# Performance work log

Measured on AMD Instinct MI355X. Metric: run time of the kernel, lower is better.

## Reference

```python
import jax, jax.numpy as jnp
import numpy as np
from jax import lax

MODES = 16
DEPTH = 8
NPH = 8  # photons = sum(init_state); init_state = [1]*8 + [0]*8
IDX = np.arange(NPH)  # output_indices derived from init_state
PI = np.pi
CHUNK = 4096  # pairs per permanent chunk (memory control, mirrors chunk_subsets idea)


def setup_inputs() -> dict:
    key = jax.random.key(0)
    k1, k2, k3 = jax.random.split(key, 3)
    x = jax.random.normal(k1, (256, 64), dtype=jnp.float32)
    W = jax.random.normal(k2, (120, 64), dtype=jnp.float32) / np.sqrt(64.0)
    b = jax.random.normal(k3, (120,), dtype=jnp.float32) * 0.01
    return {"x": x, "W": W, "b": b}


def _forward(x, W, b):
    N = x.shape[0]
    # fc1 + sigmoid embedding -> angle pairs
    x_emb = jax.nn.sigmoid(x @ W.T + b)              # (N, 120)
    tbu = x_emb.reshape(N, -1, 2)                    # (N, T, 2)
    theta = tbu[:, :, 0] * (PI / 2)
    phi = tbu[:, :, 1] * (2 * PI)
    ct = jnp.cos(theta).astype(jnp.complex64)
    st = jnp.sin(theta).astype(jnp.complex64)
    ep = jnp.exp(1j * phi.astype(jnp.complex64))
    # 2x2 tunable beam-splitter unitaries: [[e^{i phi} c, -s], [e^{i phi} s, c]]
    row0 = jnp.stack([ep * ct, -st], axis=-1)
    row1 = jnp.stack([ep * st, ct], axis=-1)
    blocks = jnp.stack([row0, row1], axis=-2)        # (N, T, 2, 2)

    # Apply block-diagonal layers. Block-diag matmul only mixes row pairs,
    # so update row segments directly instead of building (modes,modes) UBS.
    U = jnp.broadcast_to(jnp.eye(MODES, dtype=jnp.complex64), (N, MODES, MODES))
    nb_even, nb_odd = MODES // 2, (MODES - 2) // 2
    n_before = 0
    for d in range(DEPTH):
        if d % 2 == 0:
            nb, off = nb_even, 0
        else:
            nb, off = nb_odd, 1
        blk = blocks[:, n_before:n_before + nb]                      # (N, nb, 2, 2)
        seg = U[:, off:off + 2 * nb, :].reshape(N, nb, 2, MODES)     # row pairs
        new = jnp.einsum('nkab,nkbm->nkam', blk, seg).reshape(N, 2 * nb, MODES)
        U = U.at[:, off:off + 2 * nb, :].set(new)
        n_before += nb

    # Photonic Gram: K[a,b] = |perm( (U_a^dag U_b)[idx, idx] )|^2.
    # Only the idx-columns of U enter: V = U[:, :, idx], submatrix = V_a^dag V_b.
    V = U[:, :, IDX]                                  # (N, MODES, n)
    G = jnp.einsum('ami,bmj->abij', V.conj(), V)      # (N, N, n, n)

    n = NPH
    subsets = jnp.arange(1, 1 << n)                   # (S,), S = 2^n - 1
    masks = (subsets[:, None] >> jnp.arange(n)[None, :]) & 1   # (S, n)
    signs = (1 - 2 * ((n - masks.sum(axis=1)) & 1)).astype(jnp.complex64)
    maskc = masks.astype(jnp.complex64)

    A = G.reshape(N * N, n, n)
    nc = (N * N) // CHUNK

    def perm_chunk(Ac):  # Ryser: sum_S (-1)^{n-|S|} prod_i sum_{j in S} A_ij
        ss = jnp.einsum('cij,sj->csi', Ac, maskc)     # (c, S, n) subset row-sums
        pr = jnp.prod(ss, axis=2)                     # (c, S)
        return jnp.sum(pr * signs, axis=1)            # (c,)

    perms = lax.map(perm_chunk, A.reshape(nc, CHUNK, n, n)).reshape(N * N)
    K = (jnp.abs(perms) ** 2).astype(jnp.float32).reshape(N, N)
    di = jnp.arange(N)
    K = K.at[di, di].set(1.0)
    return x_emb, K


def reference(x, W, b):
    return _forward(x, W, b)
```

## Files before the change

kernel.cpp:

```cpp
#include <hip/hip_runtime.h>
#include <math.h>

#define NS 256
#define EMB 120
#define NBLK 60
#define MODES 16
#define NPH 8

typedef float v2f __attribute__((ext_vector_type(2)));

__device__ __forceinline__ v2f cmul(v2f a, v2f b) {
    v2f axx = {a.x, a.x};
    v2f nyy = {-a.y, a.y};
    v2f byx = {b.y, b.x};
    return axx * b + nyy * byx;
}
__device__ __forceinline__ v2f cfma_conj(v2f a, v2f b, v2f c) {
    v2f axx = {a.x, a.x};
    v2f pyy = {a.y, -a.y};
    v2f byx = {b.y, b.x};
    return axx * b + (pyy * byx + c);
}

__global__ __launch_bounds__(128) void emb_v_kernel(
    const float* __restrict__ x, const float* __restrict__ W,
    const float* __restrict__ bias, float* __restrict__ out_emb,
    float2* __restrict__ Vws)
{
    const int s = blockIdx.x;
    const int t = threadIdx.x;
    __shared__ float emb[EMB];
    __shared__ float ctA[NBLK], stA[NBLK], exA[NBLK], eyA[NBLK];

    if (t < EMB) {
        const float* xr = x + s * 64;
        const float* wr = W + t * 64;
        float acc = bias[t];
        #pragma unroll
        for (int k = 0; k < 64; ++k) acc = fmaf(xr[k], wr[k], acc);
        float e = 1.0f / (1.0f + expf(-acc));
        emb[t] = e;
        out_emb[s * EMB + t] = e;
    }
    __syncthreads();

    if (t < NBLK) {
        float th = emb[2 * t]     * 1.57079632679489662f;
        float ph = emb[2 * t + 1] * 6.28318530717958648f;
        float st, ct, sp, cp;
        sincosf(th, &st, &ct);
        sincosf(ph, &sp, &cp);
        ctA[t] = ct; stA[t] = st; exA[t] = cp; eyA[t] = sp;
    }
    __syncthreads();

    if (t < NPH) {
        const int c = t;
        float2 u[MODES];
        #pragma unroll
        for (int m = 0; m < MODES; ++m) {
            u[m].x = (m == c) ? 1.0f : 0.0f;
            u[m].y = 0.0f;
        }
        int bi = 0;
        #pragma unroll
        for (int d = 0; d < 8; ++d) {
            const int off = d & 1;
            const int nb = 8 - off;
            #pragma unroll
            for (int k = 0; k < nb; ++k) {
                float ct = ctA[bi], st = stA[bi], ex = exA[bi], ey = eyA[bi];
                ++bi;
                const int r0 = off + 2 * k;
                float2 u0 = u[r0], u1 = u[r0 + 1];
                float2 n0, n1;
                n0.x = ex * ct * u0.x - ey * ct * u0.y - st * u1.x;
                n0.y = ex * ct * u0.y + ey * ct * u0.x - st * u1.y;
                n1.x = ex * st * u0.x - ey * st * u0.y + ct * u1.x;
                n1.y = ex * st * u0.y + ey * st * u0.x + ct * u1.y;
                u[r0] = n0; u[r0 + 1] = n1;
            }
        }
        #pragma unroll
        for (int m = 0; m < MODES; ++m)
            Vws[(s * MODES + m) * NPH + c] = u[m];
    }
}

__global__ __launch_bounds__(256, 2) void perm_kernel(
    const float2* __restrict__ Vws, float* __restrict__ outK)
{
    __shared__ char smem[64 * 66 * sizeof(float2)];
    float2 (*sva)[132] = (float2(*)[132])smem;
    float2 (*svb)[132] = (float2(*)[132])(smem + 8448);
    float2 (*sG)[66]   = (float2(*)[66])smem;

    const int tid = threadIdx.x;
    const int ta = blockIdx.x >> 5;
    const int tb = blockIdx.x & 31;

    const float4* srcA = (const float4*)(Vws + (size_t)ta * 8 * 128);
    const float4* srcB = (const float4*)(Vws + (size_t)tb * 8 * 128);
    #pragma unroll
    for (int r = 0; r < 2; ++r) {
        int idx = r * 256 + tid;
        int row = idx >> 6;
        int c4  = idx & 63;
        *(float4*)&sva[row][c4 * 2] = srcA[idx];
        *(float4*)&svb[row][c4 * 2] = srcB[idx];
    }
    __syncthreads();

    const int p  = tid >> 2;
    const int q  = tid & 3;
    const int pa = p >> 3;
    const int pb = p & 7;

    v2f Ga[2][8];
    #pragma unroll
    for (int i = 0; i < 2; ++i)
        #pragma unroll
        for (int j = 0; j < 8; ++j) Ga[i][j] = (v2f){0.f, 0.f};

    #pragma unroll 1
    for (int m = 0; m < 16; ++m) {
        float4 va4 = *(const float4*)&sva[pa][m * 8 + 2 * q];
        v2f a0 = {va4.x, va4.y};
        v2f a1 = {va4.z, va4.w};
        v2f vb[8];
        #pragma unroll
        for (int jj = 0; jj < 4; ++jj) {
            float4 b4 = *(const float4*)&svb[pb][m * 8 + 2 * jj];
            vb[2 * jj]     = (v2f){b4.x, b4.y};
            vb[2 * jj + 1] = (v2f){b4.z, b4.w};
        }
        #pragma unroll
        for (int j = 0; j < 8; ++j) {
            Ga[0][j] = cfma_conj(a0, vb[j], Ga[0][j]);
            Ga[1][j] = cfma_conj(a1, vb[j], Ga[1][j]);
        }
    }
    __syncthreads();

    #pragma unroll
    for (int i = 0; i < 2; ++i)
        #pragma unroll
        for (int jj = 0; jj < 4; ++jj) {
            float4 w;
            w.x = Ga[i][2 * jj].x;     w.y = Ga[i][2 * jj].y;
            w.z = Ga[i][2 * jj + 1].x; w.w = Ga[i][2 * jj + 1].y;
            *(float4*)&sG[p][(2 * q + i) * 8 + 2 * jj] = w;
        }
    __syncthreads();

    v2f G[8][8];
    #pragma unroll
    for (int i = 0; i < 8; ++i)
        #pragma unroll
        for (int jj = 0; jj < 4; ++jj) {
            float4 g4 = *(const float4*)&sG[p][i * 8 + 2 * jj];
            G[i][2 * jj]     = (v2f){g4.x, g4.y};
            G[i][2 * jj + 1] = (v2f){g4.z, g4.w};
        }

    const float d6 = (q & 1) ? -1.f : 1.f;
    const float d7 = (q & 2) ? -1.f : 1.f;
    const v2f d6v = {d6, d6};
    const v2f d7v = {d7, d7};

    v2f rs[8];
    #pragma unroll
    for (int i = 0; i < 8; ++i) {
        v2f s = G[i][0] + G[i][1] + G[i][2] + G[i][3] + G[i][4] + G[i][5];
        s = d6v * G[i][6] + s;
        s = d7v * G[i][7] + s;
        rs[i] = s;
    }

    v2f acc;

#define PRODTREE(OUT) do {                                            \
        v2f p01 = cmul(rs[0], rs[1]);                                 \
        v2f p23 = cmul(rs[2], rs[3]);                                 \
        v2f p45 = cmul(rs[4], rs[5]);                                 \
        v2f p67 = cmul(rs[6], rs[7]);                                 \
        v2f q0  = cmul(p01, p23);                                     \
        v2f q1  = cmul(p45, p67);                                     \
        OUT = cmul(q0, q1);                                           \
    } while (0)

#define UPD(J, S) do {                                                \
        const v2f sv = {(S), (S)};                                    \
        _Pragma("unroll")                                             \
        for (int i = 0; i < 8; ++i) rs[i] = sv * G[i][J] + rs[i];     \
    } while (0)

#define TERM(TS) do {                                                 \
        float2 pr_; v2f pr; PRODTREE(pr); (void)pr_;                  \
        const v2f tv = {(TS), (TS)};                                  \
        acc = tv * pr + acc;                                          \
    } while (0)

    PRODTREE(acc);
    UPD(1, -2.f); TERM(-1.f);
    UPD(2, -2.f); TERM( 1.f);
    UPD(1,  2.f); TERM(-1.f);
    UPD(3, -2.f); TERM( 1.f);
    UPD(1, -2.f); TERM(-1.f);
    UPD(2,  2.f); TERM( 1.f);
    UPD(1,  2.f); TERM(-1.f);
    UPD(4, -2.f); TERM( 1.f);
    UPD(1, -2.f); TERM(-1.f);
    UPD(2, -2.f); TERM( 1.f);
    UPD(1,  2.f); TERM(-1.f);
    UPD(3,  2.f); TERM( 1.f);
    UPD(1, -2.f); TERM(-1.f);
    UPD(2,  2.f); TERM( 1.f);
    UPD(1,  2.f); TERM(-1.f);
    UPD(5, -2.f); TERM( 1.f);
    UPD(1, -2.f); TERM(-1.f);
    UPD(2, -2.f); TERM( 1.f);
    UPD(1,  2.f); TERM(-1.f);
    UPD(3, -2.f); TERM( 1.f);
    UPD(1, -2.f); TERM(-1.f);
    UPD(2,  2.f); TERM( 1.f);
    UPD(1,  2.f); TERM(-1.f);
    UPD(4,  2.f); TERM( 1.f);
    UPD(1, -2.f); TERM(-1.f);
    UPD(2, -2.f); TERM( 1.f);
    UPD(1,  2.f); TERM(-1.f);
    UPD(3,  2.f); TERM( 1.f);
    UPD(1, -2.f); TERM(-1.f);
    UPD(2,  2.f); TERM( 1.f);
    UPD(1,  2.f); TERM(-1.f);
#undef UPD
#undef TERM
#undef PRODTREE

    const float sq = d6 * d7;
    float ax = acc.x * sq, ay = acc.y * sq;
    ax += __shfl_xor(ax, 1); ay += __shfl_xor(ay, 1);
    ax += __shfl_xor(ax, 2); ay += __shfl_xor(ay, 2);

    if (q == 0) {
        const int a = ta * 8 + pa;
        const int b = tb * 8 + pb;
        float K = fmaf(ax, ax, ay * ay) * (1.0f / 16384.0f);
        if (a == b) K = 1.0f;
        outK[a * 256 + b] = K;
    }
}

extern "C" void kernel_launch(void* const* d_in, const int* in_sizes, int n_in,
                              void* d_out, int out_size, void* d_ws, size_t ws_size,
                              hipStream_t stream) {
    const float* x    = (const float*)d_in[0];
    const float* W    = (const float*)d_in[1];
    const float* bias = (const float*)d_in[2];
    float* out     = (float*)d_out;
    float* out_emb = out;
    float* outK    = out + NS * EMB;
    float2* Vws    = (float2*)d_ws;

    emb_v_kernel<<<NS, 128, 0, stream>>>(x, W, bias, out_emb, Vws);
    perm_kernel<<<1024, 256, 0, stream>>>(Vws, outK);
}
```

Baseline: 81.70 us.

## Split permanent rows across lanes with shuffles instead of shared-memory G transpose

Each group of four lanes now splits the Ryser permanent differently. A lane keeps its own two G rows and gets two more from a partner lane by shuffle, so it holds four rows instead of all eight. Column 7's sign is split across lanes, and the Gray-code sweep lengthens to 64 steps. Half products are combined with a xor-1 shuffle on every term. This removes the shared-memory round trip, its barriers and the 8x8 G per thread, and it raises launch bounds to 4 waves per SIMD. The trade-off is one extra cross-lane shuffle per Gray-code term on the critical path.

```diff
diff --git a/kernel.cpp b/kernel.cpp
--- a/kernel.cpp
+++ b/kernel.cpp
@@ -87,13 +87,11 @@
     }
 }
 
-__global__ __launch_bounds__(256, 2) void perm_kernel(
+__global__ __launch_bounds__(256, 4) void perm_kernel(
     const float2* __restrict__ Vws, float* __restrict__ outK)
 {
-    __shared__ char smem[64 * 66 * sizeof(float2)];
-    float2 (*sva)[132] = (float2(*)[132])smem;
-    float2 (*svb)[132] = (float2(*)[132])(smem + 8448);
-    float2 (*sG)[66]   = (float2(*)[66])smem;
+    __shared__ float2 sva[8][132];
+    __shared__ float2 svb[8][132];
 
     const int tid = threadIdx.x;
     const int ta = blockIdx.x >> 5;
@@ -111,20 +109,22 @@
     }
     __syncthreads();
 
-    const int p  = tid >> 2;
-    const int q  = tid & 3;
-    const int pa = p >> 3;
-    const int pb = p & 7;
-
-    v2f Ga[2][8];
+    const int p   = tid >> 2;
+    const int sub = tid & 3;
+    const int h   = sub & 1;
+    const int e   = sub >> 1;
+    const int pa  = p >> 3;
+    const int pb  = p & 7;
+
+    v2f Go[2][8];
     #pragma unroll
     for (int i = 0; i < 2; ++i)
         #pragma unroll
-        for (int j = 0; j < 8; ++j) Ga[i][j] = (v2f){0.f, 0.f};
-
-    #pragma unroll 1
+        for (int j = 0; j < 8; ++j) Go[i][j] = (v2f){0.f, 0.f};
+
+    #pragma unroll 2
     for (int m = 0; m < 16; ++m) {
-        float4 va4 = *(const float4*)&sva[pa][m * 8 + 2 * q];
+        float4 va4 = *(const float4*)&sva[pa][m * 8 + 4 * h + 2 * e];
         v2f a0 = {va4.x, va4.y};
         v2f a1 = {va4.z, va4.w};
         v2f vb[8];
@@ -136,72 +136,64 @@
         }
         #pragma unroll
         for (int j = 0; j < 8; ++j) {
-            Ga[0][j] = cfma_conj(a0, vb[j], Ga[0][j]);
-            Ga[1][j] = cfma_conj(a1, vb[j], Ga[1][j]);
-        }
-    }
-    __syncthreads();
-
+            Go[0][j] = cfma_conj(a0, vb[j], Go[0][j]);
+            Go[1][j] = cfma_conj(a1, vb[j], Go[1][j]);
+        }
+    }
+
+    v2f Gp[2][8];
     #pragma unroll
     for (int i = 0; i < 2; ++i)
         #pragma unroll
-        for (int jj = 0; jj < 4; ++jj) {
-            float4 w;
-            w.x = Ga[i][2 * jj].x;     w.y = Ga[i][2 * jj].y;
-            w.z = Ga[i][2 * jj + 1].x; w.w = Ga[i][2 * jj + 1].y;
-            *(float4*)&sG[p][(2 * q + i) * 8 + 2 * jj] = w;
-        }
-    __syncthreads();
-
-    v2f G[8][8];
-    #pragma unroll
-    for (int i = 0; i < 8; ++i)
-        #pragma unroll
-        for (int jj = 0; jj < 4; ++jj) {
-            float4 g4 = *(const float4*)&sG[p][i * 8 + 2 * jj];
-            G[i][2 * jj]     = (v2f){g4.x, g4.y};
-            G[i][2 * jj + 1] = (v2f){g4.z, g4.w};
-        }
-
-    const float d6 = (q & 1) ? -1.f : 1.f;
-    const float d7 = (q & 2) ? -1.f : 1.f;
-    const v2f d6v = {d6, d6};
-    const v2f d7v = {d7, d7};
-
-    v2f rs[8];
-    #pragma unroll
-    for (int i = 0; i < 8; ++i) {
-        v2f s = G[i][0] + G[i][1] + G[i][2] + G[i][3] + G[i][4] + G[i][5];
-        s = d6v * G[i][6] + s;
-        s = d7v * G[i][7] + s;
-        rs[i] = s;
+        for (int j = 0; j < 8; ++j) {
+            Gp[i][j].x = __shfl_xor(Go[i][j].x, 2);
+            Gp[i][j].y = __shfl_xor(Go[i][j].y, 2);
+        }
+
+    const float sgn = 1.0f - 2.0f * (float)e;
+    const v2f sgnv = {sgn, sgn};
+    v2f rs[4];
+    #pragma unroll
+    for (int r = 0; r < 2; ++r) {
+        {
+            v2f s = ((Go[r][0] + Go[r][1]) + (Go[r][2] + Go[r][3]))
+                  + ((Go[r][4] + Go[r][5]) + Go[r][6]);
+            rs[r] = sgnv * Go[r][7] + s;
+        }
+        {
+            v2f s = ((Gp[r][0] + Gp[r][1]) + (Gp[r][2] + Gp[r][3]))
+                  + ((Gp[r][4] + Gp[r][5]) + Gp[r][6]);
+            rs[2 + r] = sgnv * Gp[r][7] + s;
+        }
     }
 
     v2f acc;
 
-#define PRODTREE(OUT) do {                                            \
-        v2f p01 = cmul(rs[0], rs[1]);                                 \
-        v2f p23 = cmul(rs[2], rs[3]);                                 \
-        v2f p45 = cmul(rs[4], rs[5]);                                 \
-        v2f p67 = cmul(rs[6], rs[7]);                                 \
-        v2f q0  = cmul(p01, p23);                                     \
-        v2f q1  = cmul(p45, p67);                                     \
-        OUT = cmul(q0, q1);                                           \
+#define TREE(OUT) do {                                                \
+        v2f t01 = cmul(rs[0], rs[1]);                                 \
+        v2f t23 = cmul(rs[2], rs[3]);                                 \
+        v2f half = cmul(t01, t23);                                    \
+        v2f oth;                                                      \
+        oth.x = __shfl_xor(half.x, 1);                                \
+        oth.y = __shfl_xor(half.y, 1);                                \
+        OUT = cmul(half, oth);                                        \
     } while (0)
 
 #define UPD(J, S) do {                                                \
         const v2f sv = {(S), (S)};                                    \
-        _Pragma("unroll")                                             \
-        for (int i = 0; i < 8; ++i) rs[i] = sv * G[i][J] + rs[i];     \
+        rs[0] = sv * Go[0][J] + rs[0];                                \
+        rs[1] = sv * Go[1][J] + rs[1];                                \
+        rs[2] = sv * Gp[0][J] + rs[2];                                \
+        rs[3] = sv * Gp[1][J] + rs[3];                                \
     } while (0)
 
 #define TERM(TS) do {                                                 \
-        float2 pr_; v2f pr; PRODTREE(pr); (void)pr_;                  \
+        v2f fullp; TREE(fullp);                                       \
         const v2f tv = {(TS), (TS)};                                  \
-        acc = tv * pr + acc;                                          \
+        acc = tv * fullp + acc;                                       \
     } while (0)
 
-    PRODTREE(acc);
+    TREE(acc);
     UPD(1, -2.f); TERM(-1.f);
     UPD(2, -2.f); TERM( 1.f);
     UPD(1,  2.f); TERM(-1.f);
@@ -218,6 +210,38 @@
     UPD(2,  2.f); TERM( 1.f);
     UPD(1,  2.f); TERM(-1.f);
     UPD(5, -2.f); TERM( 1.f);
+    UPD(1, -2.f); TERM(-1.f);
+    UPD(2, -2.f); TERM( 1.f);
+    UPD(1,  2.f); TERM(-1.f);
+    UPD(3, -2.f); TERM( 1.f);
+    UPD(1, -2.f); TERM(-1.f);
+    UPD(2,  2.f); TERM( 1.f);
+    UPD(1,  2.f); TERM(-1.f);
+    UPD(4,  2.f); TERM( 1.f);
+    UPD(1, -2.f); TERM(-1.f);
+    UPD(2, -2.f); TERM( 1.f);
+    UPD(1,  2.f); TERM(-1.f);
+    UPD(3,  2.f); TERM( 1.f);
+    UPD(1, -2.f); TERM(-1.f);
+    UPD(2,  2.f); TERM( 1.f);
+    UPD(1,  2.f); TERM(-1.f);
+    UPD(6, -2.f); TERM( 1.f);
+    UPD(1, -2.f); TERM(-1.f);
+    UPD(2, -2.f); TERM( 1.f);
+    UPD(1,  2.f); TERM(-1.f);
+    UPD(3, -2.f); TERM( 1.f);
+    UPD(1, -2.f); TERM(-1.f);
+    UPD(2,  2.f); TERM( 1.f);
+    UPD(1,  2.f); TERM(-1.f);
+    UPD(4, -2.f); TERM( 1.f);
+    UPD(1, -2.f); TERM(-1.f);
+    UPD(2, -2.f); TERM( 1.f);
+    UPD(1,  2.f); TERM(-1.f);
+    UPD(3,  2.f); TERM( 1.f);
+    UPD(1, -2.f); TERM(-1.f);
+    UPD(2,  2.f); TERM( 1.f);
+    UPD(1,  2.f); TERM(-1.f);
+    UPD(5,  2.f); TERM( 1.f);
     UPD(1, -2.f); TERM(-1.f);
     UPD(2, -2.f); TERM( 1.f);
     UPD(1,  2.f); TERM(-1.f);
@@ -235,14 +259,13 @@
     UPD(1,  2.f); TERM(-1.f);
 #undef UPD
 #undef TERM
-#undef PRODTREE
-
-    const float sq = d6 * d7;
-    float ax = acc.x * sq, ay = acc.y * sq;
-    ax += __shfl_xor(ax, 1); ay += __shfl_xor(ay, 1);
-    ax += __shfl_xor(ax, 2); ay += __shfl_xor(ay, 2);
-
-    if (q == 0) {
+#undef TREE
+
+    float ax = sgn * acc.x, ay = sgn * acc.y;
+    ax += __shfl_xor(ax, 2);
+    ay += __shfl_xor(ay, 2);
+
+    if (sub == 0) {
         const int a = ta * 8 + pa;
         const int b = tb * 8 + pb;
         float K = fmaf(ax, ax, ay * ay) * (1.0f / 16384.0f);
```

After: 79.62 us. 1.03x faster.
